# Optimization experiments

Measured on AMD Instinct MI355X. Metric: run time of the kernel, lower is better.

The kernel has to match this reference:

```python
import jax, jax.numpy as jnp
import numpy as np

N_ATOMS = 20
N_IN, N_EMB_N, N_EMB_E, N_H_N, N_H_E = 4, 128, 128, 256, 256


def lstm_seq(x, Wi, bi, Wh, bh):
    """x: [B, M, T, D] -> h sequence [B, M, T, H]. Gates stacked as (i,f,g,o).
    Equivalent to the per-gate nn.Linear pairs: bi/bh are the two bias vectors."""
    B, M, T, D = x.shape
    H = Wh.shape[0]
    # precompute all input-to-hidden projections in one big GEMM: [T,B,M,4H]
    xg = jnp.einsum('bmtd,dg->tbmg', x, Wi) + bi

    def step(carry, xg_t):
        c, h = carry
        g = xg_t + h @ Wh + bh  # [B,M,4H]
        i, f, gg, o = jnp.split(g, 4, axis=-1)
        i = jax.nn.sigmoid(i)
        f = jax.nn.sigmoid(f)
        gg = jnp.tanh(gg)
        o = jax.nn.sigmoid(o)
        c = f * c + i * gg
        h = o * jnp.tanh(c)
        return (c, h), h

    z = jnp.zeros((B, M, H), x.dtype)
    _, hs = jax.lax.scan(step, (z, z), xg)  # hs: [T,B,M,H]
    return jnp.transpose(hs, (1, 2, 0, 3))


def setup_inputs() -> dict:
    key = jax.random.key(0)
    ks = jax.random.split(key, 16)
    s = 0.05
    # fully-connected directed edges without self loops -> one-hot incidence
    send, rec = np.where(~np.eye(N_ATOMS, dtype=bool))
    eye = np.eye(N_ATOMS, dtype=np.float32)
    inp = {
        'X': jax.random.normal(ks[0], (16, N_ATOMS, 64, N_IN), jnp.float32),
        'rel_rec': jnp.asarray(eye[rec]),
        'rel_send': jnp.asarray(eye[send]),
        # motion embedding fc
        'Wm': jax.random.normal(ks[1], (N_IN, N_EMB_N), jnp.float32) * s,
        'bm': jnp.zeros((N_EMB_N,), jnp.float32),
        # motion LSTM (gates i,f,g,o stacked)
        'Wmi': jax.random.normal(ks[2], (N_EMB_N, 4 * N_H_N), jnp.float32) * s,
        'bmi': jnp.zeros((4 * N_H_N,), jnp.float32),
        'Wmh': jax.random.normal(ks[3], (N_H_N, 4 * N_H_N), jnp.float32) * s,
        'bmh': jnp.zeros((4 * N_H_N,), jnp.float32),
        # interaction embedding fc (in = 2*n_h_node)
        'We': jax.random.normal(ks[4], (2 * N_H_N, N_EMB_E), jnp.float32) * s,
        'be': jnp.zeros((N_EMB_E,), jnp.float32),
        # edge LSTM
        'Wei': jax.random.normal(ks[5], (N_EMB_E, 4 * N_H_E), jnp.float32) * s,
        'bei': jnp.zeros((4 * N_H_E,), jnp.float32),
        'Weh': jax.random.normal(ks[6], (N_H_E, 4 * N_H_E), jnp.float32) * s,
        'beh': jnp.zeros((4 * N_H_E,), jnp.float32),
        # output fc
        'Wf': jax.random.normal(ks[7], (N_H_E, 1), jnp.float32) * s,
        'bf': jnp.zeros((1,), jnp.float32),
    }
    return inp


def reference(X, rel_rec, rel_send, Wm, bm, Wmi, bmi, Wmh, bmh,
              We, be, Wei, bei, Weh, beh, Wf, bf):
    # Motion embedding on temporal deltas: [B,N,T-1,n_emb_node]
    dX = X[:, :, 1:, :] - X[:, :, :-1, :]
    em = dX @ Wm + bm
    # Motion LSTM, full sequence: [B,N,T-1,Hn]
    hm = lstm_seq(em, Wmi, bmi, Wmh, bmh)
    # Interaction embedding: gather per-edge sender/receiver node states
    senders = jnp.einsum('en,bnth->beth', rel_send, hm)
    receivers = jnp.einsum('en,bnth->beth', rel_rec, hm)
    edges = jnp.concatenate([senders, receivers], axis=-1)  # [B,E,T-1,2Hn]
    ea = edges @ We + be  # [B,E,T-1,n_emb_edge]
    # Edge LSTM, last hidden state: [B,E,He]
    he = lstm_seq(ea, Wei, bei, Weh, beh)[:, :, -1, :]
    # Edge scores -> dense adjacency via incidence matrices
    A = jax.nn.sigmoid(he @ Wf + bf)[..., 0]  # [B,E]
    Ad = jnp.einsum('en,be,em->bnm', rel_send, A, rel_rec)  # send^T diag(A) rec
    return 0.5 * (Ad + jnp.transpose(Ad, (0, 2, 1)))  # symmetrize
```

## Files before the change

### kernel.cpp

```cpp
#include <hip/hip_runtime.h>
#include <stdint.h>

#define NBATCH 16
#define NNODE  20
#define TSTEPS 63
#define NEDGE  380
#define HID    256
#define RS     280
#define SPIN_MAX (1u << 20)
#define POISON  0xAAAAAAAAAAAAAAAAull

typedef __bf16 bf16x8 __attribute__((ext_vector_type(8)));
typedef float  f32x4  __attribute__((ext_vector_type(4)));

__device__ __forceinline__ float bf2f(unsigned short u){
  union { unsigned int i; float f; } v; v.i = ((unsigned int)u) << 16; return v.f;
}
__device__ __forceinline__ unsigned short f2bf(float f){
  union { float f; unsigned int i; } v; v.f = f;
  return (unsigned short)((v.i + 0x7FFFu + ((v.i >> 16) & 1u)) >> 16);
}
__device__ __forceinline__ bf16x8 as_frag(uint4 v){
  union { uint4 u; bf16x8 b; } c; c.u = v; return c.b;
}
__device__ __forceinline__ float sigmf(float x){ return 1.0f/(1.0f+__expf(-x)); }
__device__ __forceinline__ float tanh_f(float x){ float e=__expf(2.0f*x); return (e-1.0f)/(e+1.0f); }

__device__ __forceinline__ unsigned long long load_ax(const unsigned long long* p){
  return __hip_atomic_load(p, __ATOMIC_RELAXED, __HIP_MEMORY_SCOPE_AGENT);
}
__device__ __forceinline__ void store_ax(unsigned long long* p, unsigned long long v){
  __hip_atomic_store(p, v, __ATOMIC_RELAXED, __HIP_MEMORY_SCOPE_AGENT);
}

__device__ __forceinline__ void xpose4(f32x4& v, int cl){
  float s0 = __shfl_xor((float)v[1], 1), s1 = __shfl_xor((float)v[0], 1);
  float s2 = __shfl_xor((float)v[3], 1), s3 = __shfl_xor((float)v[2], 1);
  bool b0 = (cl & 1);
  float a0 = b0 ? s0 : v[0], a1 = b0 ? v[1] : s1;
  float a2 = b0 ? s2 : v[2], a3 = b0 ? v[3] : s3;
  float t0 = __shfl_xor(a2, 2), t1 = __shfl_xor(a3, 2);
  float t2 = __shfl_xor(a0, 2), t3 = __shfl_xor(a1, 2);
  bool b1 = (cl & 2);
  v[0] = b1 ? t0 : a0; v[1] = b1 ? t1 : a1;
  v[2] = b1 ? a2 : t2; v[3] = b1 ? a3 : t3;
}

__global__ __launch_bounds__(256) void prep_a(
    const float* __restrict__ We, const float* __restrict__ Wei,
    const float* __restrict__ Wm, const float* __restrict__ Wmi,
    const float* __restrict__ bm, const float* __restrict__ bmi, const float* __restrict__ bmh,
    const float* __restrict__ be, const float* __restrict__ bei, const float* __restrict__ beh,
    float* __restrict__ Wse, float* __restrict__ Wre, float* __restrict__ WcmGI,
    float* __restrict__ bcmGI, float* __restrict__ bceGI,
    float* __restrict__ Afin, uint4* __restrict__ hb3q, uint4* __restrict__ mb3q){
  int bid = blockIdx.x, tid = threadIdx.x;
  if (bid < 2048){
    int idx = bid*256 + tid;
    int half = idx >> 18;
    int j = idx & 262143;
    int k = j >> 10, nn = j & 1023;
    const float* Wrow = We + (half*256 + k)*128;
    float s = 0.f;
    for (int d = 0; d < 128; ++d) s += Wrow[d] * Wei[d*1024 + nn];
    (half ? Wre : Wse)[k*1024 + nn] = s;
  } else if (bid < 2064){
    int idx = (bid-2048)*256 + tid;
    int d = idx >> 10, ci = idx & 1023;
    int col = (ci & 3)*256 + (ci >> 2);
    float s = 0.f;
    for (int j = 0; j < 128; ++j) s += Wm[d*128 + j] * Wmi[j*1024 + col];
    WcmGI[idx] = s;
  } else if (bid < 2068){
    int ci = (bid-2064)*256 + tid;
    int col = (ci & 3)*256 + (ci >> 2);
    float s = bmi[col] + bmh[col];
    for (int j = 0; j < 128; ++j) s += bm[j] * Wmi[j*1024 + col];
    bcmGI[ci] = s;
  } else if (bid < 2072){
    int ci = (bid-2068)*256 + tid;
    int col = (ci & 3)*256 + (ci >> 2);
    float s = bei[col] + beh[col];
    for (int j = 0; j < 128; ++j) s += be[j] * Wei[j*1024 + col];
    bceGI[ci] = s;
  } else if (bid < 2096){
    int idx = (bid-2072)*256 + tid;
    if (idx < NBATCH*NEDGE) Afin[idx] = 0.f;
  } else {
    int idx = (bid-2096)*256 + tid;
    uint4 P = make_uint4(0xAAAAAAAAu,0xAAAAAAAAu,0xAAAAAAAAu,0xAAAAAAAAu);
    if (idx < 589824) hb3q[idx] = P;
    else if (idx < 638976) mb3q[idx-589824] = P;
  }
}

__device__ __forceinline__ void pack_gi(const float* __restrict__ W,
                                        unsigned short* __restrict__ dst, int id){
  int lane = id & 63, kt = (id >> 6) & 7, tt = (id >> 9) & 1, w = (id >> 10) & 7, nb = id >> 13;
  int cl = lane & 15, q = lane >> 4;
  int gcol = (cl & 3)*256 + nb*64 + (w*2 + tt)*4 + (cl >> 2);
  int k0 = kt*32 + q*8;
  unsigned int wb[4];
  #pragma unroll
  for (int p = 0; p < 4; ++p){
    unsigned short a = f2bf(W[(k0+2*p  )*1024 + gcol]);
    unsigned short b = f2bf(W[(k0+2*p+1)*1024 + gcol]);
    wb[p] = (unsigned int)a | ((unsigned int)b << 16);
  }
  ((uint4*)dst)[id] = make_uint4(wb[0], wb[1], wb[2], wb[3]);
}

__device__ __forceinline__ void pack_one(const float* __restrict__ S,
                                         unsigned short* __restrict__ dst, int id, int n){
  int lane = id & 63, kt = (id >> 6) & 7;
  int k0 = kt*32 + ((lane >> 4) << 3);
  unsigned int wb[4];
  #pragma unroll
  for (int p = 0; p < 4; ++p){
    unsigned short a = f2bf(S[(k0+2*p  )*1024 + n]);
    unsigned short b = f2bf(S[(k0+2*p+1)*1024 + n]);
    wb[p] = (unsigned int)a | ((unsigned int)b << 16);
  }
  ((uint4*)dst)[id] = make_uint4(wb[0], wb[1], wb[2], wb[3]);
}

__global__ __launch_bounds__(256) void prep_b(
    const float* __restrict__ Wmh, const float* __restrict__ Weh,
    const float* __restrict__ Wse, const float* __restrict__ Wre,
    unsigned short* __restrict__ pWmh, unsigned short* __restrict__ pWeh,
    unsigned short* __restrict__ pWsr){
  int gid = blockIdx.x*256 + threadIdx.x;
  if (gid < 32768){
    pack_gi(Wmh, pWmh, gid);
  } else if (gid < 65536){
    pack_gi(Weh, pWeh, gid - 32768);
  } else {
    int id = gid - 65536;
    int ng = (id >> 9)*16 + (id & 15);
    const float* S = (ng < 1024) ? Wse : Wre;
    pack_one(S, pWsr, id, ng & 1023);
  }
}

__global__ __launch_bounds__(512, 2) void motion_lstm(
    const float* __restrict__ X, const float* __restrict__ WcmGI,
    const float* __restrict__ bcmGI, const unsigned short* __restrict__ pWmh,
    unsigned short* __restrict__ hm, unsigned long long* __restrict__ mb3){
  __shared__ __align__(16) unsigned short hst[16*RS];
  __shared__ float dxs[10*252];
  __shared__ __align__(16) float sWc[4*256];
  __shared__ __align__(16) float sbc[256];
  int tid = threadIdx.x, lane = tid & 63, w = tid >> 6;
  int l15 = lane & 15, quad = lane >> 4;
  int m = blockIdx.x & 31, n = blockIdx.x >> 5;
  int s0 = m*10;

  uint4 wreg[2][8];
  #pragma unroll
  for (int tt = 0; tt < 2; ++tt)
    #pragma unroll
    for (int kt = 0; kt < 8; ++kt)
      wreg[tt][kt] = ((const uint4*)pWmh)[(((n*8 + w)*2 + tt)*8 + kt)*64 + lane];

  uint4 z4 = make_uint4(0,0,0,0);
  for (int i = tid; i < 560; i += 512) ((uint4*)hst)[i] = z4;
  for (int i = tid; i < 1024; i += 512) sWc[i] = WcmGI[(i >> 8)*1024 + n*256 + (i & 255)];
  if (tid < 256) sbc[tid] = bcmGI[n*256 + tid];
  for (int i = tid; i < 2520; i += 512){
    int sl = i / 252; int r = i % 252; int t = r >> 2; int d = r & 3;
    const float* Xp = X + (((size_t)(s0 + sl)*64 + t)*4 + d);
    dxs[i] = Xp[4] - Xp[0];
  }
  __syncthreads();

  float bb[2] = { sbc[(w*2+0)*16 + l15], sbc[(w*2+1)*16 + l15] };
  int row = quad*4 + (l15 & 3);
  int hsub = l15 >> 2;
  int slr = row < 10 ? row : 9;
  float ce[2] = {0.f, 0.f};

  for (int t = 0; t < TSTEPS; ++t){
    if (t > 0){
      const unsigned long long* mbp = mb3 + ((size_t)((t-1)%3)*32 + m)*1024;
      unsigned long long pv[2]; int off[2], po[2] = {-1,-1};
      #pragma unroll
      for (int j = 0; j < 2; ++j){
        int i = tid + j*512;
        if (i < 768){
          int which = i >> 8, jj = i & 255;
          int r = jj >> 4, c = jj & 15;
          int np = which + (which >= n ? 1 : 0);
          off[j] = r*64 + np*16 + c;
          po[j]  = r*RS + np*64 + c*4;
          pv[j]  = POISON;
        }
      }
      unsigned int guard = 0; bool need = true;
      while (need){
        need = false;
        #pragma unroll
        for (int j = 0; j < 2; ++j)
          if (po[j] >= 0 && pv[j] == POISON) pv[j] = load_ax(&mbp[off[j]]);
        #pragma unroll
        for (int j = 0; j < 2; ++j)
          if (po[j] >= 0 && pv[j] == POISON) need = true;
        if (need){
          if (++guard > SPIN_MAX) break;
          __builtin_amdgcn_s_sleep(1);
        }
      }
      #pragma unroll
      for (int j = 0; j < 2; ++j)
        if (po[j] >= 0) *(unsigned long long*)&hst[po[j]] = pv[j];
      if (t >= 2 && tid < 256){
        unsigned long long* mbq = mb3 + ((size_t)((t-2)%3)*32 + m)*1024;
        store_ax(&mbq[(size_t)(tid>>4)*64 + n*16 + (tid&15)], POISON);
      }
    }
    __syncthreads();

    f32x4 acc[2];
    acc[0] = (f32x4){bb[0],bb[0],bb[0],bb[0]};
    acc[1] = (f32x4){bb[1],bb[1],bb[1],bb[1]};
    #pragma unroll
    for (int kt = 0; kt < 8; ++kt){
      bf16x8 a = as_frag(*(const uint4*)&hst[l15*RS + kt*32 + quad*8]);
      acc[0] = __builtin_amdgcn_mfma_f32_16x16x32_bf16(a, as_frag(wreg[0][kt]), acc[0], 0, 0, 0);
      acc[1] = __builtin_amdgcn_mfma_f32_16x16x32_bf16(a, as_frag(wreg[1][kt]), acc[1], 0, 0, 0);
    }
    __syncthreads();

    f32x4 dxv = *(const f32x4*)&dxs[slr*252 + t*4];
    #pragma unroll
    for (int tt = 0; tt < 2; ++tt){
      int tl = w*2 + tt;
      f32x4 v = acc[tt];
      xpose4(v, l15);
      #pragma unroll
      for (int d = 0; d < 4; ++d){
        f32x4 wv = *(const f32x4*)&sWc[d*256 + tl*16 + hsub*4];
        v[0] += dxv[d]*wv[0]; v[1] += dxv[d]*wv[1];
        v[2] += dxv[d]*wv[2]; v[3] += dxv[d]*wv[3];
      }
      float iv = sigmf(v[0]), fv = sigmf(v[1]), gg = tanh_f(v[2]), ov = sigmf(v[3]);
      float cc = fv*ce[tt] + iv*gg; ce[tt] = cc;
      hst[row*RS + n*64 + tl*4 + hsub] = f2bf(ov*tanh_f(cc));
    }
    __syncthreads();

    unsigned long long* mbc = mb3 + ((size_t)(t%3)*32 + m)*1024;
    if (tid < 256){
      int r = tid >> 4, c = tid & 15;
      unsigned long long v = *(const unsigned long long*)&hst[r*RS + n*64 + c*4];
      if (t < 62) store_ax(&mbc[(size_t)r*64 + n*16 + c], v);
      if (r < 10){
        int seq = s0 + r;
        int b2 = seq / 20, nd = seq - b2*20;
        *(unsigned long long*)&hm[(((size_t)(b2*63 + t)*20) + nd)*256 + n*64 + c*4] = v;
      }
    }
  }
}

__global__ __launch_bounds__(256) void gsr_gemm(
    const unsigned short* __restrict__ hm, const unsigned short* __restrict__ pWsr,
    unsigned short* __restrict__ gsrT){
  __shared__ __align__(16) unsigned short scol[128*100];
  int tid = threadIdx.x, lane = tid & 63, wid = tid >> 6;
  int l15 = lane & 15, quad = lane >> 4;
  int bm = blockIdx.x % 252, bn = blockIdx.x / 252;
  int rowbase = bm*80;
  f32x4 acc[5][2] = {};
  #pragma unroll
  for (int kt = 0; kt < 8; ++kt){
    bf16x8 af[5];
    #pragma unroll
    for (int mt = 0; mt < 5; ++mt)
      af[mt] = as_frag(*(const uint4*)&hm[(size_t)(rowbase + mt*16 + l15)*256 + kt*32 + quad*8]);
    #pragma unroll
    for (int j = 0; j < 2; ++j){
      int ntg = bn*8 + wid*2 + j;
      bf16x8 bfr = as_frag(*(const uint4*)&pWsr[(((size_t)ntg*8 + kt)*64 + lane)*8]);
      #pragma unroll
      for (int mt = 0; mt < 5; ++mt)
        acc[mt][j] = __builtin_amdgcn_mfma_f32_16x16x32_bf16(af[mt], bfr, acc[mt][j], 0, 0, 0);
    }
  }
  #pragma unroll
  for (int mt = 0; mt < 5; ++mt)
    #pragma unroll
    for (int j = 0; j < 2; ++j){
      int colL = (wid*2 + j)*16 + l15;
      unsigned int p0 = (unsigned)f2bf(acc[mt][j][0]) | ((unsigned)f2bf(acc[mt][j][1]) << 16);
      unsigned int p1 = (unsigned)f2bf(acc[mt][j][2]) | ((unsigned)f2bf(acc[mt][j][3]) << 16);
      *(uint2*)&scol[colL*100 + mt*16 + quad*4] = make_uint2(p0, p1);
    }
  __syncthreads();
  int recv = bn >> 3;
  #pragma unroll
  for (int rep = 0; rep < 2; ++rep){
    int i = tid + rep*256;
    int btl = i >> 7, colL = i & 127;
    const unsigned short* sp = &scol[colL*100 + btl*20];
    uint2 u0 = *(const uint2*)(sp);
    uint2 u1 = *(const uint2*)(sp+4);
    uint2 u2 = *(const uint2*)(sp+8);
    uint2 u3 = *(const uint2*)(sp+12);
    uint2 u4 = *(const uint2*)(sp+16);
    unsigned short* dp = gsrT + ((size_t)(bm*4 + btl)*1024 + (bn&7)*128 + colL)*40;
    if (recv){
      *(uint4*)(dp)      = make_uint4(u0.x, u0.y, u1.x, u1.y);
      *(uint4*)(dp + 8)  = make_uint4(u2.x, u2.y, u3.x, u3.y);
      *(uint2*)(dp + 16) = u4;
    } else {
      unsigned short* dq = dp + 20;
      *(uint2*)(dq)      = u0;
      *(uint2*)(dq + 4)  = u1;
      *(uint2*)(dq + 8)  = u2;
      *(uint2*)(dq + 12) = u3;
      *(uint2*)(dq + 16) = u4;
    }
  }
}

__device__ __forceinline__ void stage_gxb(const unsigned short* __restrict__ gsrT,
                                          unsigned short* __restrict__ gx,
                                          int tid, int b, int smin, int n, int tq){
  const unsigned short* base = gsrT + (size_t)(b*63 + tq)*1024*40;
  int c = tid >> 1, chv = tid & 1;
  int g = c >> 6, hh = c & 63;
  const unsigned short* src = base + (size_t)((g << 8) + (n << 6) + hh)*40;
  unsigned short* dst = gx + (hh >> 2)*640 + (((hh & 3) << 2) + g)*40;
  if (chv == 0){
    *(uint4*)(dst)      = *(const uint4*)(src);
    *(uint4*)(dst + 8)  = *(const uint4*)(src + 8);
    *(uint2*)(dst + 16) = *(const uint2*)(src + 16);
  } else {
    const unsigned short* s3 = src + 20 + smin;
    dst[24]=s3[0]; dst[25]=s3[1]; dst[26]=s3[2]; dst[27]=s3[3]; dst[28]=s3[4];
  }
}

__global__ __launch_bounds__(512, 2) void edge_lstm(
    const unsigned short* __restrict__ gsrT, const float* __restrict__ bceGI,
    const unsigned short* __restrict__ pWeh, const float* __restrict__ Wf,
    unsigned long long* __restrict__ hb3, float* __restrict__ Afin){
  __shared__ __align__(16) unsigned short hst[96*RS];
  __shared__ __align__(16) unsigned short gxb[2][10240];
  __shared__ __align__(16) float sbce[256];
  __shared__ __align__(16) float sWf[64];
  int tid = threadIdx.x, lane = tid & 63, w = tid >> 6;
  int l15 = lane & 15, quad = lane >> 4;
  int bid = blockIdx.x;
  int n = bid >> 6, G = bid & 63, b = G >> 2, m = G & 3;
  int e0 = m*95;

  uint4 wreg[2][8];
  #pragma unroll
  for (int tt = 0; tt < 2; ++tt)
    #pragma unroll
    for (int kt = 0; kt < 8; ++kt)
      wreg[tt][kt] = ((const uint4*)pWeh)[(((n*8 + w)*2 + tt)*8 + kt)*64 + lane];

  uint4 aoh[6];
  #pragma unroll
  for (int mt = 0; mt < 6; ++mt){
    int row = mt*16 + l15;
    int e = e0 + (row < 95 ? row : 94);
    int s = e / 19; int rr = e - s*19;
    int sr = s - m*5;
    int rc = rr + (rr >= s ? 1 : 0);
    unsigned int wd[4];
    #pragma unroll
    for (int p = 0; p < 4; ++p){
      int k0 = quad*8 + 2*p, k1 = k0 + 1;
      unsigned short a0 = ((k0 < 20) ? (rc == k0) : (k0 >= 24 && k0 < 29 && sr == k0-24)) ? 0x3F80 : 0;
      unsigned short a1 = ((k1 < 20) ? (rc == k1) : (k1 >= 24 && k1 < 29 && sr == k1-24)) ? 0x3F80 : 0;
      wd[p] = (unsigned int)a0 | ((unsigned int)a1 << 16);
    }
    aoh[mt] = make_uint4(wd[0], wd[1], wd[2], wd[3]);
  }

  if (tid < 256) sbce[tid] = bceGI[n*256 + tid];
  if (tid < 64)  sWf[tid]  = Wf[n*64 + tid];
  uint4 z4 = make_uint4(0,0,0,0);
  for (int i = tid; i < 3360; i += 512) ((uint4*)hst)[i] = z4;
  for (int i = tid; i < 2560; i += 512) ((uint4*)gxb)[i] = z4;
  __syncthreads();
  stage_gxb(gsrT, &gxb[0][0], tid, b, m*5, n, 0);
  __syncthreads();

  float bb[2]  = { sbce[(w*2+0)*16 + l15], sbce[(w*2+1)*16 + l15] };
  float wfr[2] = { sWf[(w*2+0)*4 + (l15>>2)], sWf[(w*2+1)*4 + (l15>>2)] };

  float ce[2][6]; float epi[6];
  #pragma unroll
  for (int mt = 0; mt < 6; ++mt){ ce[0][mt] = 0.f; ce[1][mt] = 0.f; epi[mt] = 0.f; }

  for (int t = 0; t < TSTEPS; ++t){
    int par = t & 1, nxt = par ^ 1;
    if (t > 0){
      const unsigned long long* hbp = hb3 + ((size_t)((t-1)%3)*64 + G)*6144;
      unsigned long long pv[9]; int off[9]; int po[9];
      #pragma unroll
      for (int j = 0; j < 9; ++j){
        int i = tid + j*512;
        int which = i / 1536, jj = i - which*1536;
        int r = jj >> 4, c = jj & 15;
        int np = which + (which >= n ? 1 : 0);
        off[j] = r*64 + np*16 + c;
        po[j]  = r*RS + np*64 + c*4;
        pv[j]  = POISON;
      }
      unsigned int guard = 0; bool need = true;
      while (need){
        need = false;
        #pragma unroll
        for (int j = 0; j < 9; ++j)
          if (pv[j] == POISON) pv[j] = load_ax(&hbp[off[j]]);
        #pragma unroll
        for (int j = 0; j < 9; ++j)
          if (pv[j] == POISON) need = true;
        if (need){
          if (++guard > SPIN_MAX) break;
          __builtin_amdgcn_s_sleep(1);
        }
      }
      #pragma unroll
      for (int j = 0; j < 9; ++j)
        *(unsigned long long*)&hst[po[j]] = pv[j];
      if (t >= 2){
        unsigned long long* hbq = hb3 + ((size_t)((t-2)%3)*64 + G)*6144;
        #pragma unroll
        for (int j = 0; j < 3; ++j){
          int i = tid + j*512;
          store_ax(&hbq[(size_t)(i>>4)*64 + n*16 + (i&15)], POISON);
        }
      }
    }
    if (t + 1 < TSTEPS)
      stage_gxb(gsrT, &gxb[nxt][0], tid, b, m*5, n, t+1);
    __syncthreads();

    f32x4 acc[2][6];
    #pragma unroll
    for (int mt = 0; mt < 6; ++mt){
      acc[0][mt] = (f32x4){bb[0],bb[0],bb[0],bb[0]};
      acc[1][mt] = (f32x4){bb[1],bb[1],bb[1],bb[1]};
    }
    #pragma unroll
    for (int kt = 0; kt < 8; ++kt){
      bf16x8 a[6];
      #pragma unroll
      for (int mt = 0; mt < 6; ++mt)
        a[mt] = as_frag(*(const uint4*)&hst[(mt*16 + l15)*RS + kt*32 + quad*8]);
      #pragma unroll
      for (int mt = 0; mt < 6; ++mt){
        acc[0][mt] = __builtin_amdgcn_mfma_f32_16x16x32_bf16(a[mt], as_frag(wreg[0][kt]), acc[0][mt], 0, 0, 0);
        acc[1][mt] = __builtin_amdgcn_mfma_f32_16x16x32_bf16(a[mt], as_frag(wreg[1][kt]), acc[1][mt], 0, 0, 0);
      }
    }
    {
      bf16x8 bx0 = as_frag(*(const uint4*)&gxb[par][(w*2+0)*640 + l15*40 + quad*8]);
      bf16x8 bx1 = as_frag(*(const uint4*)&gxb[par][(w*2+1)*640 + l15*40 + quad*8]);
      #pragma unroll
      for (int mt = 0; mt < 6; ++mt){
        acc[0][mt] = __builtin_amdgcn_mfma_f32_16x16x32_bf16(as_frag(aoh[mt]), bx0, acc[0][mt], 0, 0, 0);
        acc[1][mt] = __builtin_amdgcn_mfma_f32_16x16x32_bf16(as_frag(aoh[mt]), bx1, acc[1][mt], 0, 0, 0);
      }
    }
    __syncthreads();

    #pragma unroll
    for (int tt = 0; tt < 2; ++tt){
      int tl = w*2 + tt;
      #pragma unroll
      for (int mt = 0; mt < 6; ++mt){
        f32x4 v = acc[tt][mt];
        xpose4(v, l15);
        float iv = sigmf(v[0]), fv = sigmf(v[1]), gg = tanh_f(v[2]), ov = sigmf(v[3]);
        float cc = fv*ce[tt][mt] + iv*gg; ce[tt][mt] = cc;
        float h = ov*tanh_f(cc);
        if (t < 62){
          int row = mt*16 + quad*4 + (l15 & 3);
          hst[row*RS + n*64 + tl*4 + (l15>>2)] = f2bf(h);
        } else {
          epi[mt] += h * wfr[tt];
        }
      }
    }
    if (t < 62){
      __syncthreads();
      unsigned long long* hbc = hb3 + ((size_t)(t%3)*64 + G)*6144;
      #pragma unroll
      for (int j = 0; j < 3; ++j){
        int i = tid + j*512;
        unsigned long long v = *(const unsigned long long*)&hst[(i>>4)*RS + n*64 + (i&15)*4];
        store_ax(&hbc[(size_t)(i>>4)*64 + n*16 + (i&15)], v);
      }
    }
  }
  #pragma unroll
  for (int mt = 0; mt < 6; ++mt){
    float v = epi[mt];
    v += __shfl_xor(v, 4);
    v += __shfl_xor(v, 8);
    if (l15 < 4){
      int row = mt*16 + quad*4 + l15;
      if (row < 95)
        atomicAdd(&Afin[b*380 + e0 + row], v);
    }
  }
}

__global__ __launch_bounds__(256) void finalize(const float* __restrict__ Afin,
                                                const float* __restrict__ bfp,
                                                float* __restrict__ out){
  int idx = blockIdx.x*256 + threadIdx.x;
  if (idx >= 16*400) return;
  int b = idx / 400; int ij = idx % 400; int i = ij / 20; int j = ij % 20;
  float v = 0.f;
  if (i != j){
    int e1 = i*19 + j - (j > i ? 1 : 0);
    int e2 = j*19 + i - (i > j ? 1 : 0);
    float bf = bfp[0];
    v = 0.5f*(sigmf(Afin[b*380 + e1] + bf) + sigmf(Afin[b*380 + e2] + bf));
  }
  out[idx] = v;
}

extern "C" void kernel_launch(void* const* d_in, const int* in_sizes, int n_in,
                              void* d_out, int out_size, void* d_ws, size_t ws_size,
                              hipStream_t stream){
  (void)in_sizes; (void)n_in; (void)out_size; (void)ws_size;
  const float* X   = (const float*)d_in[0];
  const float* Wm  = (const float*)d_in[3];
  const float* bm  = (const float*)d_in[4];
  const float* Wmi = (const float*)d_in[5];
  const float* bmi = (const float*)d_in[6];
  const float* Wmh = (const float*)d_in[7];
  const float* bmh = (const float*)d_in[8];
  const float* We  = (const float*)d_in[9];
  const float* be  = (const float*)d_in[10];
  const float* Wei = (const float*)d_in[11];
  const float* bei = (const float*)d_in[12];
  const float* Weh = (const float*)d_in[13];
  const float* beh = (const float*)d_in[14];
  const float* Wf  = (const float*)d_in[15];
  const float* bfp = (const float*)d_in[16];

  char* ws = (char*)d_ws;
  float* Wse   = (float*)(ws + 0);
  float* Wre   = (float*)(ws + 1048576);
  float* WcmGI = (float*)(ws + 2097152);
  float* bcmGI = (float*)(ws + 2113536);
  float* bceGI = (float*)(ws + 2117632);
  unsigned short* pWmh = (unsigned short*)(ws + 2121728);
  unsigned short* pWeh = (unsigned short*)(ws + 2646016);
  unsigned short* pWsr = (unsigned short*)(ws + 3170304);
  unsigned short* hm   = (unsigned short*)(ws + 4218880);
  unsigned short* gsrT = (unsigned short*)(ws + 14540800);
  unsigned long long* hb3 = (unsigned long long*)(ws + 97116160);
  float* Afin          = (float*)(ws + 106553344);
  unsigned long long* mb3 = (unsigned long long*)gsrT;
  float* out = (float*)d_out;

  hipLaunchKernelGGL(prep_a, dim3(4592), dim3(256), 0, stream,
                     We, Wei, Wm, Wmi, bm, bmi, bmh, be, bei, beh,
                     Wse, Wre, WcmGI, bcmGI, bceGI, Afin,
                     (uint4*)hb3, (uint4*)mb3);
  hipLaunchKernelGGL(prep_b, dim3(512), dim3(256), 0, stream,
                     Wmh, Weh, Wse, Wre, pWmh, pWeh, pWsr);
  {
    void* margs[] = {(void*)&X, (void*)&WcmGI, (void*)&bcmGI, (void*)&pWmh,
                     (void*)&hm, (void*)&mb3};
    hipLaunchCooperativeKernel(reinterpret_cast<void*>(motion_lstm),
                               dim3(128), dim3(512), margs, 0, stream);
  }
  hipLaunchKernelGGL(gsr_gemm, dim3(252*16), dim3(256), 0, stream,
                     hm, pWsr, gsrT);
  {
    void* eargs[] = {(void*)&gsrT, (void*)&bceGI, (void*)&pWeh, (void*)&Wf,
                     (void*)&hb3, (void*)&Afin};
    hipLaunchCooperativeKernel(reinterpret_cast<void*>(edge_lstm),
                               dim3(256), dim3(512), eargs, 0, stream);
  }
  hipLaunchKernelGGL(finalize, dim3(25), dim3(256), 0, stream,
                     Afin, bfp, out);
}
```

Before: 1.066 ms.

## Use FP8 recurrent weights so each edge-LSTM block owns all hidden units

The edge LSTM previously split the hidden dimension across 4 cooperative blocks per edge group and exchanged hidden states every timestep through global memory with poison-value spin waits. The recurrent weights are now quantized to FP8 with scaling, which makes them small enough for one block to hold the full 256-wide Weh in registers. Each block then processes 32 edges independently with a local double-buffered FP8 hidden state, and the cross-block exchange and the cooperative launch are removed. This trades lower recurrent precision (FP8 h and W, scaled by 8 and 64) for no inter-block synchronization, at the cost of fewer rows per MFMA tile and 192 blocks instead of 256.

New measurement: 1.248 ms. 17.0% more time.

```diff
diff --git a/kernel.cpp b/kernel.cpp
--- a/kernel.cpp
+++ b/kernel.cpp
@@ -7,21 +7,22 @@
 #define NEDGE  380
 #define HID    256
 #define RS     280
+#define RS8    272
 #define SPIN_MAX (1u << 20)
 #define POISON  0xAAAAAAAAAAAAAAAAull
 
 typedef __bf16 bf16x8 __attribute__((ext_vector_type(8)));
 typedef float  f32x4  __attribute__((ext_vector_type(4)));
 
-__device__ __forceinline__ float bf2f(unsigned short u){
-  union { unsigned int i; float f; } v; v.i = ((unsigned int)u) << 16; return v.f;
-}
 __device__ __forceinline__ unsigned short f2bf(float f){
   union { float f; unsigned int i; } v; v.f = f;
   return (unsigned short)((v.i + 0x7FFFu + ((v.i >> 16) & 1u)) >> 16);
 }
 __device__ __forceinline__ bf16x8 as_frag(uint4 v){
   union { uint4 u; bf16x8 b; } c; c.u = v; return c.b;
+}
+__device__ __forceinline__ long as_l(uint2 v){
+  union { uint2 u; long l; } c; c.u = v; return c.l;
 }
 __device__ __forceinline__ float sigmf(float x){ return 1.0f/(1.0f+__expf(-x)); }
 __device__ __forceinline__ float tanh_f(float x){ float e=__expf(2.0f*x); return (e-1.0f)/(e+1.0f); }
@@ -53,7 +54,7 @@
     const float* __restrict__ be, const float* __restrict__ bei, const float* __restrict__ beh,
     float* __restrict__ Wse, float* __restrict__ Wre, float* __restrict__ WcmGI,
     float* __restrict__ bcmGI, float* __restrict__ bceGI,
-    float* __restrict__ Afin, uint4* __restrict__ hb3q, uint4* __restrict__ mb3q){
+    float* __restrict__ Afin, uint4* __restrict__ mb3q){
   int bid = blockIdx.x, tid = threadIdx.x;
   if (bid < 2048){
     int idx = bid*256 + tid;
@@ -82,15 +83,14 @@
     int col = (ci & 3)*256 + (ci >> 2);
     float s = bei[col] + beh[col];
     for (int j = 0; j < 128; ++j) s += be[j] * Wei[j*1024 + col];
-    bceGI[ci] = s;
+    bceGI[ci] = s * 64.0f;
   } else if (bid < 2096){
     int idx = (bid-2072)*256 + tid;
     if (idx < NBATCH*NEDGE) Afin[idx] = 0.f;
   } else {
     int idx = (bid-2096)*256 + tid;
-    uint4 P = make_uint4(0xAAAAAAAAu,0xAAAAAAAAu,0xAAAAAAAAu,0xAAAAAAAAu);
-    if (idx < 589824) hb3q[idx] = P;
-    else if (idx < 638976) mb3q[idx-589824] = P;
+    if (idx < 49152)
+      mb3q[idx] = make_uint4(0xAAAAAAAAu,0xAAAAAAAAu,0xAAAAAAAAu,0xAAAAAAAAu);
   }
 }
 
@@ -110,6 +110,22 @@
   ((uint4*)dst)[id] = make_uint4(wb[0], wb[1], wb[2], wb[3]);
 }
 
+__device__ __forceinline__ void pack_fp8(const float* __restrict__ W,
+                                         unsigned int* __restrict__ dst8, int id){
+  int lane = id & 63, kt = (id >> 6) & 7, T = id >> 9;
+  int cl = lane & 15, q = lane >> 4;
+  int gcol = (cl & 3)*256 + T*4 + (cl >> 2);
+  int k0 = kt*32 + q*8;
+  float v[8];
+  #pragma unroll
+  for (int p = 0; p < 8; ++p) v[p] = W[(size_t)(k0+p)*1024 + gcol] * 8.0f;
+  unsigned int b0 = __builtin_amdgcn_cvt_pk_fp8_f32(v[0], v[1], 0, false);
+  b0 = __builtin_amdgcn_cvt_pk_fp8_f32(v[2], v[3], b0, true);
+  unsigned int b1 = __builtin_amdgcn_cvt_pk_fp8_f32(v[4], v[5], 0, false);
+  b1 = __builtin_amdgcn_cvt_pk_fp8_f32(v[6], v[7], b1, true);
+  ((uint2*)dst8)[id] = make_uint2(b0, b1);
+}
+
 __device__ __forceinline__ void pack_one(const float* __restrict__ S,
                                          unsigned short* __restrict__ dst, int id, int n){
   int lane = id & 63, kt = (id >> 6) & 7;
@@ -127,13 +143,13 @@
 __global__ __launch_bounds__(256) void prep_b(
     const float* __restrict__ Wmh, const float* __restrict__ Weh,
     const float* __restrict__ Wse, const float* __restrict__ Wre,
-    unsigned short* __restrict__ pWmh, unsigned short* __restrict__ pWeh,
+    unsigned short* __restrict__ pWmh, unsigned int* __restrict__ pWeh8,
     unsigned short* __restrict__ pWsr){
   int gid = blockIdx.x*256 + threadIdx.x;
   if (gid < 32768){
     pack_gi(Wmh, pWmh, gid);
   } else if (gid < 65536){
-    pack_gi(Weh, pWeh, gid - 32768);
+    pack_fp8(Weh, pWeh8, gid - 32768);
   } else {
     int id = gid - 65536;
     int ng = (id >> 9)*16 + (id & 15);
@@ -291,8 +307,8 @@
     #pragma unroll
     for (int j = 0; j < 2; ++j){
       int colL = (wid*2 + j)*16 + l15;
-      unsigned int p0 = (unsigned)f2bf(acc[mt][j][0]) | ((unsigned)f2bf(acc[mt][j][1]) << 16);
-      unsigned int p1 = (unsigned)f2bf(acc[mt][j][2]) | ((unsigned)f2bf(acc[mt][j][3]) << 16);
+      unsigned int p0 = (unsigned)f2bf(acc[mt][j][0]*64.f) | ((unsigned)f2bf(acc[mt][j][1]*64.f) << 16);
+      unsigned int p1 = (unsigned)f2bf(acc[mt][j][2]*64.f) | ((unsigned)f2bf(acc[mt][j][3]*64.f) << 16);
       *(uint2*)&scol[colL*100 + mt*16 + quad*4] = make_uint2(p0, p1);
     }
   __syncthreads();
@@ -323,191 +339,142 @@
   }
 }
 
-__device__ __forceinline__ void stage_gxb(const unsigned short* __restrict__ gsrT,
-                                          unsigned short* __restrict__ gx,
-                                          int tid, int b, int smin, int n, int tq){
-  const unsigned short* base = gsrT + (size_t)(b*63 + tq)*1024*40;
-  int c = tid >> 1, chv = tid & 1;
-  int g = c >> 6, hh = c & 63;
-  const unsigned short* src = base + (size_t)((g << 8) + (n << 6) + hh)*40;
-  unsigned short* dst = gx + (hh >> 2)*640 + (((hh & 3) << 2) + g)*40;
-  if (chv == 0){
-    *(uint4*)(dst)      = *(const uint4*)(src);
-    *(uint4*)(dst + 8)  = *(const uint4*)(src + 8);
-    *(uint2*)(dst + 16) = *(const uint2*)(src + 16);
-  } else {
-    const unsigned short* s3 = src + 20 + smin;
-    dst[24]=s3[0]; dst[25]=s3[1]; dst[26]=s3[2]; dst[27]=s3[3]; dst[28]=s3[4];
-  }
-}
-
-__global__ __launch_bounds__(512, 2) void edge_lstm(
+__global__ __launch_bounds__(512) void edge_lstm(
     const unsigned short* __restrict__ gsrT, const float* __restrict__ bceGI,
-    const unsigned short* __restrict__ pWeh, const float* __restrict__ Wf,
-    unsigned long long* __restrict__ hb3, float* __restrict__ Afin){
-  __shared__ __align__(16) unsigned short hst[96*RS];
-  __shared__ __align__(16) unsigned short gxb[2][10240];
-  __shared__ __align__(16) float sbce[256];
-  __shared__ __align__(16) float sWf[64];
+    const unsigned int* __restrict__ pWeh8, const float* __restrict__ Wf,
+    float* __restrict__ Afin){
+  __shared__ __align__(16) unsigned char hst8[2][32*RS8];
+  __shared__ __align__(16) unsigned short gxb[64*512];
+  __shared__ __align__(16) float sbce[1024];
+  __shared__ __align__(16) float sWf[256];
   int tid = threadIdx.x, lane = tid & 63, w = tid >> 6;
   int l15 = lane & 15, quad = lane >> 4;
-  int bid = blockIdx.x;
-  int n = bid >> 6, G = bid & 63, b = G >> 2, m = G & 3;
-  int e0 = m*95;
-
-  uint4 wreg[2][8];
-  #pragma unroll
-  for (int tt = 0; tt < 2; ++tt)
+  int b = blockIdx.x / 12, m = blockIdx.x % 12;
+  int e0 = m*32;
+  int valid = (NEDGE - e0 < 32) ? NEDGE - e0 : 32;
+  int smin = e0 / 19;
+
+  uint2 wreg[8][8];
+  #pragma unroll
+  for (int j = 0; j < 8; ++j)
     #pragma unroll
     for (int kt = 0; kt < 8; ++kt)
-      wreg[tt][kt] = ((const uint4*)pWeh)[(((n*8 + w)*2 + tt)*8 + kt)*64 + lane];
-
-  uint4 aoh[6];
-  #pragma unroll
-  for (int mt = 0; mt < 6; ++mt){
+      wreg[j][kt] = ((const uint2*)pWeh8)[((w*8 + j)*8 + kt)*64 + lane];
+
+  uint4 aoh[2];
+  #pragma unroll
+  for (int mt = 0; mt < 2; ++mt){
     int row = mt*16 + l15;
-    int e = e0 + (row < 95 ? row : 94);
+    int e = e0 + (row < valid ? row : valid-1);
     int s = e / 19; int rr = e - s*19;
-    int sr = s - m*5;
+    int sr = s - smin;
     int rc = rr + (rr >= s ? 1 : 0);
     unsigned int wd[4];
     #pragma unroll
     for (int p = 0; p < 4; ++p){
       int k0 = quad*8 + 2*p, k1 = k0 + 1;
-      unsigned short a0 = ((k0 < 20) ? (rc == k0) : (k0 >= 24 && k0 < 29 && sr == k0-24)) ? 0x3F80 : 0;
-      unsigned short a1 = ((k1 < 20) ? (rc == k1) : (k1 >= 24 && k1 < 29 && sr == k1-24)) ? 0x3F80 : 0;
+      unsigned short a0 = ((k0 < 20) ? (rc == k0) : (k0 >= 24 && k0 < 27 && sr == k0-24)) ? 0x3F80 : 0;
+      unsigned short a1 = ((k1 < 20) ? (rc == k1) : (k1 >= 24 && k1 < 27 && sr == k1-24)) ? 0x3F80 : 0;
       wd[p] = (unsigned int)a0 | ((unsigned int)a1 << 16);
     }
     aoh[mt] = make_uint4(wd[0], wd[1], wd[2], wd[3]);
   }
 
-  if (tid < 256) sbce[tid] = bceGI[n*256 + tid];
-  if (tid < 64)  sWf[tid]  = Wf[n*64 + tid];
   uint4 z4 = make_uint4(0,0,0,0);
-  for (int i = tid; i < 3360; i += 512) ((uint4*)hst)[i] = z4;
-  for (int i = tid; i < 2560; i += 512) ((uint4*)gxb)[i] = z4;
+  for (int i = tid; i < 1088; i += 512) ((uint4*)hst8)[i] = z4;
+  for (int i = tid; i < 8192; i += 512) ((uint4*)gxb)[i] = z4;
+  sbce[tid] = bceGI[tid]; sbce[tid+512] = bceGI[tid+512];
+  if (tid < 256) sWf[tid] = Wf[tid];
   __syncthreads();
-  stage_gxb(gsrT, &gxb[0][0], tid, b, m*5, n, 0);
+  #pragma unroll
+  for (int r = 0; r < 2; ++r){
+    int c = tid + r*512;
+    const unsigned short* rec = gsrT + ((size_t)(b*63)*1024 + c)*40;
+    unsigned short* dst = &gxb[(c >> 4)*512 + (c & 15)*32];
+    *(uint4*)(dst)      = *(const uint4*)(rec);
+    *(uint4*)(dst + 8)  = *(const uint4*)(rec + 8);
+    *(uint2*)(dst + 16) = *(const uint2*)(rec + 16);
+    dst[24] = rec[20 + smin]; dst[25] = rec[21 + smin]; dst[26] = rec[22 + smin];
+  }
   __syncthreads();
 
-  float bb[2]  = { sbce[(w*2+0)*16 + l15], sbce[(w*2+1)*16 + l15] };
-  float wfr[2] = { sWf[(w*2+0)*4 + (l15>>2)], sWf[(w*2+1)*4 + (l15>>2)] };
-
-  float ce[2][6]; float epi[6];
-  #pragma unroll
-  for (int mt = 0; mt < 6; ++mt){ ce[0][mt] = 0.f; ce[1][mt] = 0.f; epi[mt] = 0.f; }
+  float bb[8], wfr[8];
+  #pragma unroll
+  for (int j = 0; j < 8; ++j){
+    bb[j]  = sbce[(w*8 + j)*16 + l15];
+    wfr[j] = sWf[(w*8 + j)*4 + (l15 >> 2)];
+  }
+  float ce[2][8]; float epi[2] = {0.f, 0.f};
+  #pragma unroll
+  for (int mt = 0; mt < 2; ++mt)
+    #pragma unroll
+    for (int j = 0; j < 8; ++j) ce[mt][j] = 0.f;
 
   for (int t = 0; t < TSTEPS; ++t){
     int par = t & 1, nxt = par ^ 1;
-    if (t > 0){
-      const unsigned long long* hbp = hb3 + ((size_t)((t-1)%3)*64 + G)*6144;
-      unsigned long long pv[9]; int off[9]; int po[9];
-      #pragma unroll
-      for (int j = 0; j < 9; ++j){
-        int i = tid + j*512;
-        int which = i / 1536, jj = i - which*1536;
-        int r = jj >> 4, c = jj & 15;
-        int np = which + (which >= n ? 1 : 0);
-        off[j] = r*64 + np*16 + c;
-        po[j]  = r*RS + np*64 + c*4;
-        pv[j]  = POISON;
-      }
-      unsigned int guard = 0; bool need = true;
-      while (need){
-        need = false;
-        #pragma unroll
-        for (int j = 0; j < 9; ++j)
-          if (pv[j] == POISON) pv[j] = load_ax(&hbp[off[j]]);
-        #pragma unroll
-        for (int j = 0; j < 9; ++j)
-          if (pv[j] == POISON) need = true;
-        if (need){
-          if (++guard > SPIN_MAX) break;
-          __builtin_amdgcn_s_sleep(1);
-        }
-      }
-      #pragma unroll
-      for (int j = 0; j < 9; ++j)
-        *(unsigned long long*)&hst[po[j]] = pv[j];
-      if (t >= 2){
-        unsigned long long* hbq = hb3 + ((size_t)((t-2)%3)*64 + G)*6144;
-        #pragma unroll
-        for (int j = 0; j < 3; ++j){
-          int i = tid + j*512;
-          store_ax(&hbq[(size_t)(i>>4)*64 + n*16 + (i&15)], POISON);
-        }
-      }
-    }
-    if (t + 1 < TSTEPS)
-      stage_gxb(gsrT, &gxb[nxt][0], tid, b, m*5, n, t+1);
+    f32x4 acc[2][8];
+    #pragma unroll
+    for (int mt = 0; mt < 2; ++mt)
+      #pragma unroll
+      for (int j = 0; j < 8; ++j) acc[mt][j] = (f32x4){bb[j], bb[j], bb[j], bb[j]};
+    #pragma unroll
+    for (int kt = 0; kt < 8; ++kt){
+      long a0 = as_l(*(const uint2*)&hst8[par][(     l15)*RS8 + kt*32 + quad*8]);
+      long a1 = as_l(*(const uint2*)&hst8[par][(16 + l15)*RS8 + kt*32 + quad*8]);
+      #pragma unroll
+      for (int j = 0; j < 8; ++j){
+        acc[0][j] = __builtin_amdgcn_mfma_f32_16x16x32_fp8_fp8(a0, as_l(wreg[j][kt]), acc[0][j], 0, 0, 0);
+        acc[1][j] = __builtin_amdgcn_mfma_f32_16x16x32_fp8_fp8(a1, as_l(wreg[j][kt]), acc[1][j], 0, 0, 0);
+      }
+    }
+    #pragma unroll
+    for (int j = 0; j < 8; ++j){
+      bf16x8 bx = as_frag(*(const uint4*)&gxb[(w*8 + j)*512 + l15*32 + quad*8]);
+      acc[0][j] = __builtin_amdgcn_mfma_f32_16x16x32_bf16(as_frag(aoh[0]), bx, acc[0][j], 0, 0, 0);
+      acc[1][j] = __builtin_amdgcn_mfma_f32_16x16x32_bf16(as_frag(aoh[1]), bx, acc[1][j], 0, 0, 0);
+    }
     __syncthreads();
-
-    f32x4 acc[2][6];
-    #pragma unroll
-    for (int mt = 0; mt < 6; ++mt){
-      acc[0][mt] = (f32x4){bb[0],bb[0],bb[0],bb[0]};
-      acc[1][mt] = (f32x4){bb[1],bb[1],bb[1],bb[1]};
-    }
-    #pragma unroll
-    for (int kt = 0; kt < 8; ++kt){
-      bf16x8 a[6];
-      #pragma unroll
-      for (int mt = 0; mt < 6; ++mt)
-        a[mt] = as_frag(*(const uint4*)&hst[(mt*16 + l15)*RS + kt*32 + quad*8]);
-      #pragma unroll
-      for (int mt = 0; mt < 6; ++mt){
-        acc[0][mt] = __builtin_amdgcn_mfma_f32_16x16x32_bf16(a[mt], as_frag(wreg[0][kt]), acc[0][mt], 0, 0, 0);
-        acc[1][mt] = __builtin_amdgcn_mfma_f32_16x16x32_bf16(a[mt], as_frag(wreg[1][kt]), acc[1][mt], 0, 0, 0);
-      }
-    }
-    {
-      bf16x8 bx0 = as_frag(*(const uint4*)&gxb[par][(w*2+0)*640 + l15*40 + quad*8]);
-      bf16x8 bx1 = as_frag(*(const uint4*)&gxb[par][(w*2+1)*640 + l15*40 + quad*8]);
-      #pragma unroll
-      for (int mt = 0; mt < 6; ++mt){
-        acc[0][mt] = __builtin_amdgcn_mfma_f32_16x16x32_bf16(as_frag(aoh[mt]), bx0, acc[0][mt], 0, 0, 0);
-        acc[1][mt] = __builtin_amdgcn_mfma_f32_16x16x32_bf16(as_frag(aoh[mt]), bx1, acc[1][mt], 0, 0, 0);
-      }
-    }
-    __syncthreads();
-
-    #pragma unroll
-    for (int tt = 0; tt < 2; ++tt){
-      int tl = w*2 + tt;
-      #pragma unroll
-      for (int mt = 0; mt < 6; ++mt){
-        f32x4 v = acc[tt][mt];
+    if (t + 1 < TSTEPS){
+      #pragma unroll
+      for (int r = 0; r < 2; ++r){
+        int c = tid + r*512;
+        const unsigned short* rec = gsrT + ((size_t)(b*63 + t + 1)*1024 + c)*40;
+        unsigned short* dst = &gxb[(c >> 4)*512 + (c & 15)*32];
+        *(uint4*)(dst)      = *(const uint4*)(rec);
+        *(uint4*)(dst + 8)  = *(const uint4*)(rec + 8);
+        *(uint2*)(dst + 16) = *(const uint2*)(rec + 16);
+        dst[24] = rec[20 + smin]; dst[25] = rec[21 + smin]; dst[26] = rec[22 + smin];
+      }
+    }
+    #pragma unroll
+    for (int j = 0; j < 8; ++j){
+      #pragma unroll
+      for (int mt = 0; mt < 2; ++mt){
+        f32x4 v = acc[mt][j];
+        v[0] *= 0.015625f; v[1] *= 0.015625f; v[2] *= 0.015625f; v[3] *= 0.015625f;
         xpose4(v, l15);
         float iv = sigmf(v[0]), fv = sigmf(v[1]), gg = tanh_f(v[2]), ov = sigmf(v[3]);
-        float cc = fv*ce[tt][mt] + iv*gg; ce[tt][mt] = cc;
+        float cc = fv*ce[mt][j] + iv*gg; ce[mt][j] = cc;
         float h = ov*tanh_f(cc);
         if (t < 62){
+          unsigned int q = __builtin_amdgcn_cvt_pk_fp8_f32(h*8.0f, h*8.0f, 0, false);
           int row = mt*16 + quad*4 + (l15 & 3);
-          hst[row*RS + n*64 + tl*4 + (l15>>2)] = f2bf(h);
+          hst8[nxt][row*RS8 + (w*8 + j)*4 + (l15 >> 2)] = (unsigned char)q;
         } else {
-          epi[mt] += h * wfr[tt];
+          epi[mt] += h * wfr[j];
         }
       }
     }
-    if (t < 62){
-      __syncthreads();
-      unsigned long long* hbc = hb3 + ((size_t)(t%3)*64 + G)*6144;
-      #pragma unroll
-      for (int j = 0; j < 3; ++j){
-        int i = tid + j*512;
-        unsigned long long v = *(const unsigned long long*)&hst[(i>>4)*RS + n*64 + (i&15)*4];
-        store_ax(&hbc[(size_t)(i>>4)*64 + n*16 + (i&15)], v);
-      }
-    }
-  }
-  #pragma unroll
-  for (int mt = 0; mt < 6; ++mt){
+    __syncthreads();
+  }
+  #pragma unroll
+  for (int mt = 0; mt < 2; ++mt){
     float v = epi[mt];
     v += __shfl_xor(v, 4);
     v += __shfl_xor(v, 8);
     if (l15 < 4){
       int row = mt*16 + quad*4 + l15;
-      if (row < 95)
+      if (row < valid)
         atomicAdd(&Afin[b*380 + e0 + row], v);
     }
   }
@@ -556,21 +523,19 @@
   float* bcmGI = (float*)(ws + 2113536);
   float* bceGI = (float*)(ws + 2117632);
   unsigned short* pWmh = (unsigned short*)(ws + 2121728);
-  unsigned short* pWeh = (unsigned short*)(ws + 2646016);
+  unsigned int* pWeh8  = (unsigned int*)(ws + 2646016);
   unsigned short* pWsr = (unsigned short*)(ws + 3170304);
   unsigned short* hm   = (unsigned short*)(ws + 4218880);
   unsigned short* gsrT = (unsigned short*)(ws + 14540800);
-  unsigned long long* hb3 = (unsigned long long*)(ws + 97116160);
-  float* Afin          = (float*)(ws + 106553344);
+  float* Afin          = (float*)(ws + 97116160);
   unsigned long long* mb3 = (unsigned long long*)gsrT;
   float* out = (float*)d_out;
 
-  hipLaunchKernelGGL(prep_a, dim3(4592), dim3(256), 0, stream,
+  hipLaunchKernelGGL(prep_a, dim3(2288), dim3(256), 0, stream,
                      We, Wei, Wm, Wmi, bm, bmi, bmh, be, bei, beh,
-                     Wse, Wre, WcmGI, bcmGI, bceGI, Afin,
-                     (uint4*)hb3, (uint4*)mb3);
+                     Wse, Wre, WcmGI, bcmGI, bceGI, Afin, (uint4*)mb3);
   hipLaunchKernelGGL(prep_b, dim3(512), dim3(256), 0, stream,
-                     Wmh, Weh, Wse, Wre, pWmh, pWeh, pWsr);
+                     Wmh, Weh, Wse, Wre, pWmh, pWeh8, pWsr);
   {
     void* margs[] = {(void*)&X, (void*)&WcmGI, (void*)&bcmGI, (void*)&pWmh,
                      (void*)&hm, (void*)&mb3};
@@ -579,12 +544,8 @@
   }
   hipLaunchKernelGGL(gsr_gemm, dim3(252*16), dim3(256), 0, stream,
                      hm, pWsr, gsrT);
-  {
-    void* eargs[] = {(void*)&gsrT, (void*)&bceGI, (void*)&pWeh, (void*)&Wf,
-                     (void*)&hb3, (void*)&Afin};
-    hipLaunchCooperativeKernel(reinterpret_cast<void*>(edge_lstm),
-                               dim3(256), dim3(512), eargs, 0, stream);
-  }
+  hipLaunchKernelGGL(edge_lstm, dim3(192), dim3(512), 0, stream,
+                     gsrT, bceGI, pWeh8, Wf, Afin);
   hipLaunchKernelGGL(finalize, dim3(25), dim3(256), 0, stream,
                      Afin, bfp, out);
 }
```
